# Kernel optimization log

Measured on AMD Instinct MI355X. Metric: run time of the kernel, lower is better.

Reference implementation:

```python
import jax, jax.numpy as jnp
import numpy as np

V_PATCH_NUMS = (1, 2, 3, 4, 5, 6, 8, 10, 13, 16)


def _pool_matrix(in_size: int, out_size: int) -> jnp.ndarray:
    # Matrix form of torch adaptive_avg_pool1d (== F.interpolate mode='area'):
    # window i averages input bins [floor(i*in/out), ceil((i+1)*in/out)).
    M = np.zeros((out_size, in_size), dtype=np.float32)
    for i in range(out_size):
        s = (i * in_size) // out_size
        e = -((-(i + 1) * in_size) // out_size)  # ceil division
        M[i, s:e] = 1.0 / (e - s)
    return jnp.asarray(M)


def setup_inputs() -> dict:
    key = jax.random.key(0)
    k1, k2 = jax.random.split(key)
    B, C, H, W = 64, 32, 16, 16
    vocab = 4096
    f = jax.random.normal(k1, (B, C, H, W), dtype=jnp.float32)
    # embedding init: uniform(-1/vocab, 1/vocab), as in the torch module
    emb = (jax.random.uniform(k2, (vocab, C), dtype=jnp.float32) * 2.0 - 1.0) / vocab
    return {"f": f, "emb": emb}


def reference(f, emb):
    # Multi-scale residual VQ: per scale -> area-downsample residual,
    # nearest-codebook argmin, embedding gather, bicubic-upsample,
    # accumulate into f_hat and subtract from f_rest.
    B, C, H, W = f.shape
    f = jax.lax.stop_gradient(f)            # f_no_grad in torch
    x = jnp.transpose(f, (0, 2, 3, 1))      # BHWC for resize/gather
    f_rest = x
    f_hat = jnp.zeros_like(x)
    emb_ng = jax.lax.stop_gradient(emb)     # distances use embedding.weight.data
    e_sq = jnp.sum(emb_ng * emb_ng, axis=1)  # [vocab]
    SN = len(V_PATCH_NUMS)
    for si, pn in enumerate(V_PATCH_NUMS):
        last = si == SN - 1
        if last:
            z = f_rest                       # [B,H,W,C]
        else:
            Mh = _pool_matrix(H, pn)
            Mw = _pool_matrix(W, pn)
            z = jnp.einsum('ph,qw,bhwc->bpqc', Mh, Mw, f_rest)  # area interp
        z_NC = z.reshape(-1, C)
        # squared L2 distance to every code: ||z||^2 + ||e||^2 - 2 z e^T
        d = jnp.sum(z_NC * z_NC, axis=1, keepdims=True) + e_sq - 2.0 * (z_NC @ emb_ng.T)
        idx = jnp.argmin(d, axis=1).reshape(B, pn, pn)
        h = emb[idx]                         # [B,pn,pn,C] gather (grad-carrying emb)
        if not last:
            h = jax.image.resize(h, (B, H, W, C), method='cubic')  # bicubic up
        f_hat = f_hat + h
        f_rest = f_rest - h
    return jnp.transpose(f_hat, (0, 3, 1, 2))  # back to BCHW
```

## Files before the change

kernel.cpp:

```cpp
#include <hip/hip_runtime.h>
#include <math.h>

#define WS_ESQ   0
#define WS_STATE 4096
#define WS_FHAT  (4096 + 524288)
#define WS_Z     (4096 + 2*524288)
#define WS_PSC   (4096 + 3*524288)

__device__ __forceinline__ float4 v4add(float4 a, float4 b) {
    return make_float4(__fadd_rn(a.x,b.x), __fadd_rn(a.y,b.y),
                       __fadd_rn(a.z,b.z), __fadd_rn(a.w,b.w));
}
__device__ __forceinline__ float4 v4sq(float4 a) {
    return make_float4(__fmul_rn(a.x,a.x), __fmul_rn(a.y,a.y),
                       __fmul_rn(a.z,a.z), __fmul_rn(a.w,a.w));
}
__device__ __forceinline__ float np_pw32(float4 q0, float4 q1, float4 q2, float4 q3,
                                         float4 q4, float4 q5, float4 q6, float4 q7) {
    float4 rA = v4add(v4add(v4add(q0, q2), q4), q6);
    float4 rB = v4add(v4add(v4add(q1, q3), q5), q7);
    float l = __fadd_rn(__fadd_rn(rA.x, rA.y), __fadd_rn(rA.z, rA.w));
    float h = __fadd_rn(__fadd_rn(rB.x, rB.y), __fadd_rn(rB.z, rB.w));
    return __fadd_rn(l, h);
}

__device__ __forceinline__ double keys64(double x) {
    if (x < 1.0)      return ((1.5*x - 2.5)*x)*x + 1.0;
    else if (x < 2.0) return ((-0.5*x + 2.5)*x - 4.0)*x + 2.0;
    return 0.0;
}

__global__ __launch_bounds__(256) void vq_apply(
    const float* __restrict__ f, const float* __restrict__ emb,
    float* __restrict__ esq, float* __restrict__ state, float* __restrict__ fhat,
    float* __restrict__ zws, const unsigned long long* __restrict__ keysPrev,
    unsigned long long* __restrict__ keysCur,
    int sIdx, int pn, int pnPrev)
{
    __shared__ float fr[1280];
    __shared__ float hs[676];
    __shared__ int   idx_arr[176];
    __shared__ float U[256];

    const int tid = threadIdx.x;
    const int wg  = blockIdx.x;
    if (wg >= 512) {
        int j = ((wg - 512) << 8) + tid;
        const float4* e4 = (const float4*)(emb + (size_t)j*32);
        esq[j] = np_pw32(v4sq(e4[0]),v4sq(e4[1]),v4sq(e4[2]),v4sq(e4[3]),
                         v4sq(e4[4]),v4sq(e4[5]),v4sq(e4[6]),v4sq(e4[7]));
        return;
    }
    const int b  = wg >> 3;
    const int c0 = (wg & 7) * 4;

    if ((wg & 7) == 0) {
        const int V = pn * pn;
        for (int v = tid; v < V; v += 256) keysCur[(v << 6) + b] = ~0ull;
    }

    const float* src = (sIdx <= 1) ? f : state;
    for (int o = tid; o < 1024; o += 256) {
        int cc = o >> 8, yx = o & 255;
        fr[yx*5 + cc] = src[b*8192 + (c0 + cc)*256 + yx];
    }
    __syncthreads();

    if (sIdx > 0) {
        const int Vp = pnPrev * pnPrev;
        if (tid < Vp)
            idx_arr[tid] = (int)(keysPrev[((size_t)tid << 6) + b] & 0xffffffffu);
        __syncthreads();
        for (int t = tid; t < Vp*4; t += 256)
            hs[t] = emb[(size_t)idx_arr[t >> 2]*32 + c0 + (t & 3)];
        if (tid < 16) {
            double scl = 16.0 / (double)pnPrev;
            double inv = 1.0 / scl;
            double sp = ((double)tid + 0.5) * inv - 0.5;
            double w64[16]; double tot = 0.0;
            for (int q = 0; q < pnPrev; ++q) {
                double wv = keys64(fabs(sp - (double)q));
                w64[q] = wv; tot += wv;
            }
            for (int q = 0; q < pnPrev; ++q) U[tid*16 + q] = (float)(w64[q] / tot);
        }
        __syncthreads();
        {
            const double inv = 1.0 / (16.0 / (double)pnPrev);
            const int yx = tid, y = yx >> 4, x = yx & 15;
            double sy = ((double)y + 0.5) * inv - 0.5;
            double sx = ((double)x + 0.5) * inv - 0.5;
            int p0 = (int)floor(sy) - 1, q0 = (int)floor(sx) - 1;
            int pa = max(0, p0), pb = min(pnPrev - 1, p0 + 3);
            int qa = max(0, q0), qb = min(pnPrev - 1, q0 + 3);
            float acc0 = 0.f, acc1 = 0.f, acc2 = 0.f, acc3 = 0.f;
            for (int p = pa; p <= pb; ++p) {
                float wy = U[y*16 + p];
                for (int q = qa; q <= qb; ++q) {
                    float wx = U[x*16 + q];
                    const float* hp = &hs[(p*pnPrev + q)*4];
                    acc0 = __fadd_rn(acc0, __fmul_rn(__fmul_rn(hp[0], wy), wx));
                    acc1 = __fadd_rn(acc1, __fmul_rn(__fmul_rn(hp[1], wy), wx));
                    acc2 = __fadd_rn(acc2, __fmul_rn(__fmul_rn(hp[2], wy), wx));
                    acc3 = __fadd_rn(acc3, __fmul_rn(__fmul_rn(hp[3], wy), wx));
                }
            }
            float a4[4] = {acc0, acc1, acc2, acc3};
            #pragma unroll
            for (int cc = 0; cc < 4; ++cc) {
                float frv = __fsub_rn(fr[yx*5 + cc], a4[cc]);
                fr[yx*5 + cc] = frv;
                int go = b*8192 + (c0 + cc)*256 + yx;
                state[go] = frv;
                fhat[go] = (sIdx == 1) ? a4[cc] : __fadd_rn(fhat[go], a4[cc]);
            }
        }
        __syncthreads();
    }

    const int V = pn * pn;
    if (pn < 16) {
        if (tid < V) {
            int p = tid / pn, q = tid - p*pn;
            int sh = (p*16)/pn, eh = ((p+1)*16 + pn - 1)/pn;
            int sw = (q*16)/pn, ew = ((q+1)*16 + pn - 1)/pn;
            float Mh = (float)(1.0/(double)(eh - sh));
            float Mw = (float)(1.0/(double)(ew - sw));
            float coef = __fmul_rn(Mh, Mw);
            float a4[4] = {0.f, 0.f, 0.f, 0.f};
            for (int hh = sh; hh < eh; ++hh)
                for (int wy = sw; wy < ew; ++wy) {
                    const float* fp = &fr[(hh*16 + wy)*5];
                    #pragma unroll
                    for (int cc = 0; cc < 4; ++cc)
                        a4[cc] = __fadd_rn(a4[cc], __fmul_rn(coef, fp[cc]));
                }
            *(float4*)(zws + (size_t)((tid << 6) + b)*32 + c0) =
                make_float4(a4[0], a4[1], a4[2], a4[3]);
        }
    } else {
        const int yx = tid;
        *(float4*)(zws + (size_t)((yx << 6) + b)*32 + c0) =
            make_float4(fr[yx*5], fr[yx*5 + 1], fr[yx*5 + 2], fr[yx*5 + 3]);
    }
}

typedef float f32x16 __attribute__((ext_vector_type(16)));
typedef float f32x2  __attribute__((ext_vector_type(2)));

#define SLOADW2(E0, E1, F0, F1, Q2, JS) { \
    const float* _pe = emb + ((size_t)(JS) << 5); \
    const float* _pq = esq + (JS); \
    asm volatile("s_load_dwordx16 %0, %5, 0x0\n\t" \
                 "s_load_dwordx16 %1, %5, 0x40\n\t" \
                 "s_load_dwordx16 %2, %5, 0x80\n\t" \
                 "s_load_dwordx16 %3, %5, 0xC0\n\t" \
                 "s_load_dwordx2  %4, %6, 0x0\n\t" \
                 "s_waitcnt lgkmcnt(0)" \
        : "=&s"(E0), "=&s"(E1), "=&s"(F0), "=&s"(F1), "=&s"(Q2) \
        : "s"(_pe), "s"(_pq)); }

#define DOT4S(EV, K, ZA, ZB) { \
    const float ex_ = EV[4*(K)+0], ey_ = EV[4*(K)+1]; \
    const float ez_ = EV[4*(K)+2], ew_ = EV[4*(K)+3]; \
    acc0 = __fmaf_rn(ex_, ZA.x, acc0); acc1 = __fmaf_rn(ex_, ZB.x, acc1); \
    acc0 = __fmaf_rn(ey_, ZA.y, acc0); acc1 = __fmaf_rn(ey_, ZB.y, acc1); \
    acc0 = __fmaf_rn(ez_, ZA.z, acc0); acc1 = __fmaf_rn(ez_, ZB.z, acc1); \
    acc0 = __fmaf_rn(ew_, ZA.w, acc0); acc1 = __fmaf_rn(ew_, ZB.w, acc1); }

#define CODE_STEP(E0, E1, SQ, J) { \
    float acc0 = 0.f, acc1 = 0.f; \
    DOT4S(E0, 0, a0, b0) DOT4S(E0, 1, a1, b1) DOT4S(E0, 2, a2, b2) DOT4S(E0, 3, a3, b3) \
    DOT4S(E1, 0, a4, b4) DOT4S(E1, 1, a5, b5) DOT4S(E1, 2, a6, b6) DOT4S(E1, 3, a7, b7) \
    float d0 = __fsub_rn(__fadd_rn(zsq0, SQ), __fmul_rn(2.0f, acc0)); \
    float d1 = __fsub_rn(__fadd_rn(zsq1, SQ), __fmul_rn(2.0f, acc1)); \
    if (d0 < best0) { best0 = d0; bi0 = (J); } \
    if (d1 < best1) { best1 = d1; bi1 = (J); } }

__global__ __launch_bounds__(256, 4) void vq_scan(
    const float* __restrict__ emb, const float* __restrict__ esq,
    const float* __restrict__ zws, unsigned long long* __restrict__ keys,
    int V, int PB, int CB)
{
    __shared__ float red_f[512];
    __shared__ int   red_i[512];

    const int tid  = threadIdx.x;
    const int cb   = blockIdx.x / PB;
    const int pblk = blockIdx.x - cb * PB;
    const int w    = tid >> 6, lane = tid & 63;
    const int N    = V << 6;

    const int pair0 = (pblk << 7) + lane;
    const int p0c = min(pair0, N - 1), p1c = min(pair0 + 64, N - 1);
    const float4* za = (const float4*)(zws + (size_t)p0c*32);
    const float4* zb = (const float4*)(zws + (size_t)p1c*32);
    float4 a0 = za[0], a1 = za[1], a2 = za[2], a3 = za[3];
    float4 a4 = za[4], a5 = za[5], a6 = za[6], a7 = za[7];
    float4 b0 = zb[0], b1 = zb[1], b2 = zb[2], b3 = zb[3];
    float4 b4 = zb[4], b5 = zb[5], b6 = zb[6], b7 = zb[7];
    float zsq0 = np_pw32(v4sq(a0),v4sq(a1),v4sq(a2),v4sq(a3),
                         v4sq(a4),v4sq(a5),v4sq(a6),v4sq(a7));
    float zsq1 = np_pw32(v4sq(b0),v4sq(b1),v4sq(b2),v4sq(b3),
                         v4sq(b4),v4sq(b5),v4sq(b6),v4sq(b7));

    const int jchunk = cb * CB;
    const int pw     = CB >> 2;
    const int w_u    = __builtin_amdgcn_readfirstlane(w);
    const int jbase  = jchunk + w_u * pw;

    float best0 = INFINITY, best1 = INFINITY; int bi0 = 0, bi1 = 0;
    for (int i = 0; i < pw; i += 2) {
        const int j = jbase + i;
        f32x16 e0, e1, f0, f1; f32x2 q2;
        SLOADW2(e0, e1, f0, f1, q2, j);
        const float q0 = q2[0], q1 = q2[1];
        CODE_STEP(e0, e1, q0, j);
        CODE_STEP(f0, f1, q1, j + 1);
    }

    red_f[w*128 + lane]      = best0;  red_i[w*128 + lane]      = bi0;
    red_f[w*128 + 64 + lane] = best1;  red_i[w*128 + 64 + lane] = bi1;
    __syncthreads();

    if (tid < 128) {
        const int p = (pblk << 7) + tid;
        if (p < N) {
            float bb = INFINITY; int bi = 0x7fffffff;
            #pragma unroll
            for (int ww = 0; ww < 4; ++ww) {
                float sc = red_f[ww*128 + tid];
                int   ji = red_i[ww*128 + tid];
                if (sc < bb || (sc == bb && ji < bi)) { bb = sc; bi = ji; }
            }
            unsigned u  = __float_as_uint(bb);
            unsigned mu = (u & 0x80000000u) ? ~u : (u | 0x80000000u);
            unsigned long long key =
                ((unsigned long long)mu << 32) | (unsigned long long)(unsigned)bi;
            atomicMin(&keys[p], key);
        }
    }
}

__global__ __launch_bounds__(256) void vq_final(
    const float* __restrict__ emb, const float* __restrict__ fhat,
    const unsigned long long* __restrict__ keys,
    float* __restrict__ out)
{
    __shared__ int idx_arr[256];
    const int tid = threadIdx.x;
    const int b = blockIdx.x;
    idx_arr[tid] = (int)(keys[((size_t)tid << 6) + b] & 0xffffffffu);
    __syncthreads();
    for (int o = tid; o < 8192; o += 256) {
        int c = o >> 8, yx = o & 255;
        out[b*8192 + o] = __fadd_rn(fhat[(size_t)b*8192 + o],
                                    emb[(size_t)idx_arr[yx]*32 + c]);
    }
}

extern "C" void kernel_launch(void* const* d_in, const int* in_sizes, int n_in,
                              void* d_out, int out_size, void* d_ws, size_t ws_size,
                              hipStream_t stream) {
    const float* f   = (const float*)d_in[0];
    const float* emb = (const float*)d_in[1];
    float* ws  = (float*)d_ws;
    float* out = (float*)d_out;
    float* esq   = ws + WS_ESQ;
    float* state = ws + WS_STATE;
    float* fhatp = ws + WS_FHAT;
    float* zws   = ws + WS_Z;
    unsigned long long* keysA = (unsigned long long*)(ws + WS_PSC);
    static const int pns[10] = {1, 2, 3, 4, 5, 6, 8, 10, 13, 16};
    static const int cbs[10] = {16, 16, 16, 16, 32, 32, 64, 128, 128, 256};

    for (int s = 0; s < 10; ++s) {
        int pn = pns[s], V = pn*pn, CB = cbs[s];
        int NC = 4096 / CB;
        int PB = ((V << 6) + 127) >> 7;
        unsigned long long* keysCur  = keysA + (size_t)(s & 1) * 16384;
        unsigned long long* keysPrev = keysA + (size_t)((s & 1) ^ 1) * 16384;
        vq_apply<<<(s == 0) ? 528 : 512, 256, 0, stream>>>(
            f, emb, esq, state, fhatp, zws, keysPrev, keysCur,
            s, pn, s > 0 ? pns[s-1] : 0);
        vq_scan<<<PB * NC, 256, 0, stream>>>(emb, esq, zws, keysCur, V, PB, CB);
    }
    vq_final<<<64, 256, 0, stream>>>(emb, fhatp, keysA + 16384, out);
}
```

Measured before the change: 368.1 us.

## Load codebook via vector loads with double-buffered prefetch in VQ scan

```diff
diff --git a/kernel.cpp b/kernel.cpp
--- a/kernel.cpp
+++ b/kernel.cpp
@@ -145,78 +145,99 @@
     }
 }
 
-typedef float f32x16 __attribute__((ext_vector_type(16)));
-typedef float f32x2  __attribute__((ext_vector_type(2)));
-
-#define SLOADW2(E0, E1, F0, F1, Q2, JS) { \
-    const float* _pe = emb + ((size_t)(JS) << 5); \
-    const float* _pq = esq + (JS); \
-    asm volatile("s_load_dwordx16 %0, %5, 0x0\n\t" \
-                 "s_load_dwordx16 %1, %5, 0x40\n\t" \
-                 "s_load_dwordx16 %2, %5, 0x80\n\t" \
-                 "s_load_dwordx16 %3, %5, 0xC0\n\t" \
-                 "s_load_dwordx2  %4, %6, 0x0\n\t" \
-                 "s_waitcnt lgkmcnt(0)" \
-        : "=&s"(E0), "=&s"(E1), "=&s"(F0), "=&s"(F1), "=&s"(Q2) \
-        : "s"(_pe), "s"(_pq)); }
-
-#define DOT4S(EV, K, ZA, ZB) { \
-    const float ex_ = EV[4*(K)+0], ey_ = EV[4*(K)+1]; \
-    const float ez_ = EV[4*(K)+2], ew_ = EV[4*(K)+3]; \
-    acc0 = __fmaf_rn(ex_, ZA.x, acc0); acc1 = __fmaf_rn(ex_, ZB.x, acc1); \
-    acc0 = __fmaf_rn(ey_, ZA.y, acc0); acc1 = __fmaf_rn(ey_, ZB.y, acc1); \
-    acc0 = __fmaf_rn(ez_, ZA.z, acc0); acc1 = __fmaf_rn(ez_, ZB.z, acc1); \
-    acc0 = __fmaf_rn(ew_, ZA.w, acc0); acc1 = __fmaf_rn(ew_, ZB.w, acc1); }
-
-#define CODE_STEP(E0, E1, SQ, J) { \
+#define LOADE(C0,C1,C2,C3,C4,C5,C6,C7,Q,JV) { \
+    const float4* _e4 = (const float4*)(emb + ((size_t)(unsigned)(JV) << 5)); \
+    C0 = _e4[0]; C1 = _e4[1]; C2 = _e4[2]; C3 = _e4[3]; \
+    C4 = _e4[4]; C5 = _e4[5]; C6 = _e4[6]; C7 = _e4[7]; \
+    Q  = esq[(unsigned)(JV)]; }
+
+#define DOT4V(C, ZA, ZB) { \
+    acc0 = __fmaf_rn(C.x, ZA.x, acc0); acc1 = __fmaf_rn(C.x, ZB.x, acc1); \
+    acc0 = __fmaf_rn(C.y, ZA.y, acc0); acc1 = __fmaf_rn(C.y, ZB.y, acc1); \
+    acc0 = __fmaf_rn(C.z, ZA.z, acc0); acc1 = __fmaf_rn(C.z, ZB.z, acc1); \
+    acc0 = __fmaf_rn(C.w, ZA.w, acc0); acc1 = __fmaf_rn(C.w, ZB.w, acc1); }
+
+#define CODE_STEPV(C0,C1,C2,C3,C4,C5,C6,C7,Q,J) { \
     float acc0 = 0.f, acc1 = 0.f; \
-    DOT4S(E0, 0, a0, b0) DOT4S(E0, 1, a1, b1) DOT4S(E0, 2, a2, b2) DOT4S(E0, 3, a3, b3) \
-    DOT4S(E1, 0, a4, b4) DOT4S(E1, 1, a5, b5) DOT4S(E1, 2, a6, b6) DOT4S(E1, 3, a7, b7) \
-    float d0 = __fsub_rn(__fadd_rn(zsq0, SQ), __fmul_rn(2.0f, acc0)); \
-    float d1 = __fsub_rn(__fadd_rn(zsq1, SQ), __fmul_rn(2.0f, acc1)); \
+    DOT4V(C0, za0, zb0) DOT4V(C1, za1, zb1) DOT4V(C2, za2, zb2) DOT4V(C3, za3, zb3) \
+    DOT4V(C4, za4, zb4) DOT4V(C5, za5, zb5) DOT4V(C6, za6, zb6) DOT4V(C7, za7, zb7) \
+    float d0 = __fsub_rn(__fadd_rn(zsq0, Q), __fmul_rn(2.0f, acc0)); \
+    float d1 = __fsub_rn(__fadd_rn(zsq1, Q), __fmul_rn(2.0f, acc1)); \
     if (d0 < best0) { best0 = d0; bi0 = (J); } \
     if (d1 < best1) { best1 = d1; bi1 = (J); } }
 
-__global__ __launch_bounds__(256, 4) void vq_scan(
+__global__ __launch_bounds__(256, 3) void vq_scan(
     const float* __restrict__ emb, const float* __restrict__ esq,
     const float* __restrict__ zws, unsigned long long* __restrict__ keys,
-    int V, int PB, int CB)
+    int V, int ncMask, int ncShift)
 {
     __shared__ float red_f[512];
     __shared__ int   red_i[512];
 
     const int tid  = threadIdx.x;
-    const int cb   = blockIdx.x / PB;
-    const int pblk = blockIdx.x - cb * PB;
+    const int cb   = blockIdx.x & ncMask;
+    const int pblk = blockIdx.x >> ncShift;
     const int w    = tid >> 6, lane = tid & 63;
     const int N    = V << 6;
+    const int CB   = 4096 >> ncShift;
 
     const int pair0 = (pblk << 7) + lane;
     const int p0c = min(pair0, N - 1), p1c = min(pair0 + 64, N - 1);
-    const float4* za = (const float4*)(zws + (size_t)p0c*32);
-    const float4* zb = (const float4*)(zws + (size_t)p1c*32);
-    float4 a0 = za[0], a1 = za[1], a2 = za[2], a3 = za[3];
-    float4 a4 = za[4], a5 = za[5], a6 = za[6], a7 = za[7];
-    float4 b0 = zb[0], b1 = zb[1], b2 = zb[2], b3 = zb[3];
-    float4 b4 = zb[4], b5 = zb[5], b6 = zb[6], b7 = zb[7];
-    float zsq0 = np_pw32(v4sq(a0),v4sq(a1),v4sq(a2),v4sq(a3),
-                         v4sq(a4),v4sq(a5),v4sq(a6),v4sq(a7));
-    float zsq1 = np_pw32(v4sq(b0),v4sq(b1),v4sq(b2),v4sq(b3),
-                         v4sq(b4),v4sq(b5),v4sq(b6),v4sq(b7));
+
+    float4 za0, za1, za2, za3, za4, za5, za6, za7;
+    float4 zb0, zb1, zb2, zb3, zb4, zb5, zb6, zb7;
+    {
+        unsigned long long pa = (unsigned long long)(zws + (size_t)p0c*32);
+        unsigned long long pb = (unsigned long long)(zws + (size_t)p1c*32);
+        asm volatile(
+            "global_load_dwordx4 %0, %16, off\n\t"
+            "global_load_dwordx4 %1, %16, off offset:16\n\t"
+            "global_load_dwordx4 %2, %16, off offset:32\n\t"
+            "global_load_dwordx4 %3, %16, off offset:48\n\t"
+            "global_load_dwordx4 %4, %16, off offset:64\n\t"
+            "global_load_dwordx4 %5, %16, off offset:80\n\t"
+            "global_load_dwordx4 %6, %16, off offset:96\n\t"
+            "global_load_dwordx4 %7, %16, off offset:112\n\t"
+            "global_load_dwordx4 %8, %17, off\n\t"
+            "global_load_dwordx4 %9, %17, off offset:16\n\t"
+            "global_load_dwordx4 %10, %17, off offset:32\n\t"
+            "global_load_dwordx4 %11, %17, off offset:48\n\t"
+            "global_load_dwordx4 %12, %17, off offset:64\n\t"
+            "global_load_dwordx4 %13, %17, off offset:80\n\t"
+            "global_load_dwordx4 %14, %17, off offset:96\n\t"
+            "global_load_dwordx4 %15, %17, off offset:112\n\t"
+            "s_waitcnt vmcnt(0)"
+            : "=&v"(za0), "=&v"(za1), "=&v"(za2), "=&v"(za3),
+              "=&v"(za4), "=&v"(za5), "=&v"(za6), "=&v"(za7),
+              "=&v"(zb0), "=&v"(zb1), "=&v"(zb2), "=&v"(zb3),
+              "=&v"(zb4), "=&v"(zb5), "=&v"(zb6), "=&v"(zb7)
+            : "v"(pa), "v"(pb));
+    }
+    float zsq0 = np_pw32(v4sq(za0),v4sq(za1),v4sq(za2),v4sq(za3),
+                         v4sq(za4),v4sq(za5),v4sq(za6),v4sq(za7));
+    float zsq1 = np_pw32(v4sq(zb0),v4sq(zb1),v4sq(zb2),v4sq(zb3),
+                         v4sq(zb4),v4sq(zb5),v4sq(zb6),v4sq(zb7));
 
     const int jchunk = cb * CB;
     const int pw     = CB >> 2;
     const int w_u    = __builtin_amdgcn_readfirstlane(w);
     const int jbase  = jchunk + w_u * pw;
+    const int jv0    = __shfl(jbase, 0);
+    const int jrel_max = 4095 - jbase;
+
+    float4 eA0,eA1,eA2,eA3,eA4,eA5,eA6,eA7; float qA;
+    float4 eB0,eB1,eB2,eB3,eB4,eB5,eB6,eB7; float qB;
+    LOADE(eA0,eA1,eA2,eA3,eA4,eA5,eA6,eA7,qA, jv0);
 
     float best0 = INFINITY, best1 = INFINITY; int bi0 = 0, bi1 = 0;
     for (int i = 0; i < pw; i += 2) {
-        const int j = jbase + i;
-        f32x16 e0, e1, f0, f1; f32x2 q2;
-        SLOADW2(e0, e1, f0, f1, q2, j);
-        const float q0 = q2[0], q1 = q2[1];
-        CODE_STEP(e0, e1, q0, j);
-        CODE_STEP(f0, f1, q1, j + 1);
+        LOADE(eB0,eB1,eB2,eB3,eB4,eB5,eB6,eB7,qB, jv0 + (i + 1));
+        CODE_STEPV(eA0,eA1,eA2,eA3,eA4,eA5,eA6,eA7,qA, jbase + i);
+        {
+            int jr = i + 2; if (jr > jrel_max) jr = jrel_max;
+            LOADE(eA0,eA1,eA2,eA3,eA4,eA5,eA6,eA7,qA, jv0 + jr);
+        }
+        CODE_STEPV(eB0,eB1,eB2,eB3,eB4,eB5,eB6,eB7,qB, jbase + i + 1);
     }
 
     red_f[w*128 + lane]      = best0;  red_i[w*128 + lane]      = bi0;
@@ -272,18 +293,18 @@
     float* zws   = ws + WS_Z;
     unsigned long long* keysA = (unsigned long long*)(ws + WS_PSC);
     static const int pns[10] = {1, 2, 3, 4, 5, 6, 8, 10, 13, 16};
-    static const int cbs[10] = {16, 16, 16, 16, 32, 32, 64, 128, 128, 256};
+    static const int ncs[10] = {8, 8, 8, 8, 7, 7, 6, 5, 5, 4};
 
     for (int s = 0; s < 10; ++s) {
-        int pn = pns[s], V = pn*pn, CB = cbs[s];
-        int NC = 4096 / CB;
+        int pn = pns[s], V = pn*pn, sh = ncs[s];
         int PB = ((V << 6) + 127) >> 7;
         unsigned long long* keysCur  = keysA + (size_t)(s & 1) * 16384;
         unsigned long long* keysPrev = keysA + (size_t)((s & 1) ^ 1) * 16384;
         vq_apply<<<(s == 0) ? 528 : 512, 256, 0, stream>>>(
             f, emb, esq, state, fhatp, zws, keysPrev, keysCur,
             s, pn, s > 0 ? pns[s-1] : 0);
-        vq_scan<<<PB * NC, 256, 0, stream>>>(emb, esq, zws, keysCur, V, PB, CB);
+        vq_scan<<<PB << sh, 256, 0, stream>>>(emb, esq, zws, keysCur,
+                                              V, (1 << sh) - 1, sh);
     }
     vq_final<<<64, 256, 0, stream>>>(emb, fhatp, keysA + 16384, out);
 }
```

Result: slower. 692.0 us (+88.0%).
